# Optimization experiments

Hardware: AMD Instinct MI355X
Metric: run time of the kernel (lower is better)

Reference implementation:

```python
import jax, jax.numpy as jnp
import numpy as np

BETA = 1e10  # hard softmax temperature from the original module


def setup_inputs() -> dict:
    key = jax.random.key(0)
    ks = jax.random.split(key, 7)
    bs, nc, units, feat = 128, 1024, 512, 512
    return {
        "x": jax.random.normal(ks[0], (bs, feat), jnp.float32),
        "class_logits": jax.random.normal(ks[1], (bs, nc), jnp.float32),
        "h_states": jax.random.normal(ks[2], (nc, units), jnp.float32) * 0.1,
        "c_states": jax.random.normal(ks[3], (nc, units), jnp.float32) * 0.1,
        "kernel": jax.random.normal(ks[4], (feat, 4 * units), jnp.float32) * 0.05,
        "rec_kernel": jax.random.normal(ks[5], (units, 4 * units), jnp.float32) * 0.05,
        "bias": jnp.zeros((4 * units,), jnp.float32),
    }


def _diff_scatter(A, B, w):
    # A: (nc, u) old class states, B: (bs, u) new states, w: (bs, nc) hard softmax.
    # Faithful to tf version: broadcast to (nc, bs, u), blend, then reduce_max over bs.
    m = w.T[:, :, None]                       # (nc, bs, 1)
    blended = A[:, None, :] * (1.0 - m) + B[None, :, :] * m  # (nc, bs, u)
    return jnp.max(blended, axis=1)           # (nc, u)


def reference(x, class_logits, h_states, c_states, kernel, rec_kernel, bias):
    # diff_gather: softmax-weighted sum over classes == weights @ params
    w = jax.nn.softmax(class_logits * BETA, axis=-1)  # (bs, nc), ~one-hot
    h0 = w @ h_states                                  # (bs, u)
    c0 = w @ c_states                                  # (bs, u)

    # single-step Keras LSTM (seq_len == 1): gate order i, f, c, o
    z = x @ kernel + h0 @ rec_kernel + bias            # (bs, 4u)
    i, f, g, o = jnp.split(z, 4, axis=-1)
    i = jax.nn.sigmoid(i)
    f = jax.nn.sigmoid(f)
    g = jnp.tanh(g)
    o = jax.nn.sigmoid(o)
    c = f * c0 + i * g
    h = o * jnp.tanh(c)                                # LSTM output == h

    new_h = _diff_scatter(h_states, h, w)
    new_c = _diff_scatter(c_states, c, w)
    return h, new_h, new_c
```

## Files before the change

kernel.cpp:

```cpp
#include <hip/hip_runtime.h>
#include <hip/hip_bf16.h>
#include <math.h>

#define BS    128
#define NC    1024
#define UNITS 512
#define FEAT  512
#define FOURU 2048
#define KG    8

typedef short bf16x8 __attribute__((ext_vector_type(8)));
typedef float f32x4  __attribute__((ext_vector_type(4)));

__device__ __forceinline__ unsigned short bf_rhu(float f) {
    union { float f; unsigned u; } v; v.f = f;
    return (unsigned short)((v.u + 0x8000u) >> 16);
}
__device__ __forceinline__ unsigned pack2(float a, float b) {
    return (unsigned)bf_rhu(a) | ((unsigned)bf_rhu(b) << 16);
}

__global__ __launch_bounds__(256) void prep_kernel(
    const float* __restrict__ logits, const float* __restrict__ x,
    const float* __restrict__ h_st,
    const float* __restrict__ kern, const float* __restrict__ reck,
    int* __restrict__ sidx,
    unsigned short* __restrict__ Abf,
    unsigned short* __restrict__ Wt)
{
    const int bid = blockIdx.x, t = threadIdx.x;
    const int wid = t >> 6, lane = t & 63;

    if (bid < BS) {
        int b = bid;
        float best = -INFINITY; int bi = 0;
        for (int i = t; i < NC; i += 256) {
            float v = logits[b * NC + i];
            if (v > best) { best = v; bi = i; }
        }
        for (int off = 32; off > 0; off >>= 1) {
            float ov = __shfl_down(best, off);
            int   oi = __shfl_down(bi, off);
            if (ov > best || (ov == best && oi < bi)) { best = ov; bi = oi; }
        }
        __shared__ float sv[4]; __shared__ int si[4]; __shared__ int sbi;
        if ((t & 63) == 0) { sv[wid] = best; si[wid] = bi; }
        __syncthreads();
        if (t == 0) {
            for (int w = 1; w < 4; ++w)
                if (sv[w] > best || (sv[w] == best && si[w] < bi)) { best = sv[w]; bi = si[w]; }
            sidx[b] = bi;
            sbi = bi;
        }
        __syncthreads();
        int st = t & 127;
        const float* srcrow = (t < 128) ? (x + (long)b * FEAT)
                                        : (h_st + (long)sbi * UNITS);
        float4 v = *(const float4*)(srcrow + st * 4);
        unsigned lo = pack2(v.x, v.y), hi = pack2(v.z, v.w);
        unsigned du = (unsigned)b * 512u + (t < 128 ? 0u : 256u) + (unsigned)st * 2u;
        *(uint2*)((unsigned*)Abf + du) = make_uint2(lo, hi);
    } else {
        int gw = (bid - BS) * 4 + wid;
        for (int task = gw; task < 4096; task += 1536) {
            int kc = task >> 5;
            int n  = (task & 31) * 64 + lane;
            int r0 = kc * 8;
            const float* base = (r0 < 512) ? (kern + (long)r0 * FOURU + n)
                                           : (reck + (long)(r0 - 512) * FOURU + n);
            bf16x8 o;
            #pragma unroll
            for (int j = 0; j < 8; ++j)
                o[j] = (short)bf_rhu(base[(long)j * FOURU]);
            *(bf16x8*)(Wt + (long)n * 1024 + r0) = o;
        }
    }
}

__global__ __launch_bounds__(256) void gemm_kernel(
    const unsigned short* __restrict__ Abf,
    const unsigned short* __restrict__ Wt,
    float* __restrict__ z_part)
{
    const int t = threadIdx.x;
    const int wid = t >> 6, lane = t & 63, l15 = lane & 15, quad = lane >> 4;
    const int nt = blockIdx.x & 63, kg = blockIdx.x >> 6;
    const int k0base = kg * 128 + quad * 8;

    f32x4 zero = {0.f, 0.f, 0.f, 0.f};
    f32x4 acc[2][2] = {{zero, zero}, {zero, zero}};

    #pragma unroll
    for (int kstep = 0; kstep < 4; ++kstep) {
        int k0 = k0base + kstep * 32;
        bf16x8 af[2], wf[2];
        #pragma unroll
        for (int ms = 0; ms < 2; ++ms) {
            int m = wid * 32 + ms * 16 + l15;
            af[ms] = *(const bf16x8*)(Abf + (long)m * 1024 + k0);
        }
        #pragma unroll
        for (int ns = 0; ns < 2; ++ns) {
            int n = nt * 32 + ns * 16 + l15;
            wf[ns] = *(const bf16x8*)(Wt + (long)n * 1024 + k0);
        }
        #pragma unroll
        for (int ms = 0; ms < 2; ++ms)
            #pragma unroll
            for (int ns = 0; ns < 2; ++ns)
                acc[ms][ns] = __builtin_amdgcn_mfma_f32_16x16x32_bf16(
                                  af[ms], wf[ns], acc[ms][ns], 0, 0, 0);
    }

    float* zp = z_part + (long)kg * BS * FOURU;
    #pragma unroll
    for (int ms = 0; ms < 2; ++ms)
        #pragma unroll
        for (int ns = 0; ns < 2; ++ns)
            #pragma unroll
            for (int r = 0; r < 4; ++r) {
                int m = wid * 32 + ms * 16 + quad * 4 + r;
                int n = nt * 32 + ns * 16 + l15;
                zp[(long)m * FOURU + n] = acc[ms][ns][r];
            }
}

__global__ __launch_bounds__(256) void scatter_lstm_kernel(
    const float* __restrict__ z_part, const float* __restrict__ bias,
    const float* __restrict__ h_states, const float* __restrict__ c_states,
    const int* __restrict__ sidx,
    float* __restrict__ h_out, float* __restrict__ out_h, float* __restrict__ out_c)
{
    __shared__ int s[BS];
    int t = threadIdx.x;
    if (t < BS) s[t] = sidx[t];
    __syncthreads();
    int j = blockIdx.x >> 1;
    int u = (blockIdx.x & 1) * 256 + t;

    float ah = h_states[(long)j * UNITS + u];
    float ac = c_states[(long)j * UNITS + u];

    float mh = -INFINITY, mc = -INFINITY;
    int count = 0;
    float bi_ = bias[u], bf_ = bias[512 + u], bg_ = bias[1024 + u], bo_ = bias[1536 + u];

    for (int b = 0; b < BS; ++b) {
        if (s[b] == j) {
            ++count;
            float zi = bi_, zf = bf_, zg = bg_, zo = bo_;
            #pragma unroll
            for (int kg = 0; kg < KG; ++kg) {
                const float* zp = z_part + (long)kg * BS * FOURU + (long)b * FOURU;
                zi += zp[u];
                zf += zp[512 + u];
                zg += zp[1024 + u];
                zo += zp[1536 + u];
            }
            float ig = 1.f / (1.f + expf(-zi));
            float fg = 1.f / (1.f + expf(-zf));
            float gg = tanhf(zg);
            float og = 1.f / (1.f + expf(-zo));
            float c  = fg * ac + ig * gg;
            float h  = og * tanhf(c);
            h_out[(long)b * UNITS + u] = h;
            mh = fmaxf(mh, h);
            mc = fmaxf(mc, c);
        }
    }
    out_h[(long)j * UNITS + u] = (count == BS) ? mh : fmaxf(ah, mh);
    out_c[(long)j * UNITS + u] = (count == BS) ? mc : fmaxf(ac, mc);
}

extern "C" void kernel_launch(void* const* d_in, const int* in_sizes, int n_in,
                              void* d_out, int out_size, void* d_ws, size_t ws_size,
                              hipStream_t stream)
{
    (void)in_sizes; (void)n_in; (void)out_size; (void)ws_size;
    const float* x      = (const float*)d_in[0];
    const float* logits = (const float*)d_in[1];
    const float* h_st   = (const float*)d_in[2];
    const float* c_st   = (const float*)d_in[3];
    const float* kern   = (const float*)d_in[4];
    const float* reck   = (const float*)d_in[5];
    const float* bias   = (const float*)d_in[6];

    float* out        = (float*)d_out;
    float* out_h_step = out;
    float* out_newh   = out + BS * UNITS;
    float* out_newc   = out + BS * UNITS + NC * UNITS;

    char*           ws     = (char*)d_ws;
    int*            sidx   = (int*)ws;
    unsigned short* Abf    = (unsigned short*)(ws + 4096);
    float*          z_part = (float*)(ws + (1u << 20));
    unsigned short* Wt     = (unsigned short*)(ws + 10u * (1u << 20));

    prep_kernel<<<512, 256, 0, stream>>>(logits, x, h_st, kern, reck, sidx, Abf, Wt);
    gemm_kernel<<<512, 256, 0, stream>>>(Abf, Wt, z_part);
    scatter_lstm_kernel<<<NC * UNITS / 256, 256, 0, stream>>>(
        z_part, bias, h_st, c_st, sidx, out_h_step, out_newh, out_newc);
}
```

Baseline: 103.3 us.

## Fuse weight bf16 conversion into GEMM loads and drop transposed weight buffer

Removes the separate pass that converts kernel/rec_kernel into a transposed bf16 buffer. The GEMM now reads fp32 weights directly and converts them in registers while building MFMA fragments. The grid changes to 128 N-tiles of 16 columns by 4 K-groups of 256, which halves the split-K partials the scatter kernel must sum. This saves a full write and re-read of the 8 MB weight copy, at the cost of strided fp32 loads and fewer MFMAs per loaded A fragment.

```diff
diff --git a/kernel.cpp b/kernel.cpp
--- a/kernel.cpp
+++ b/kernel.cpp
@@ -7,7 +7,8 @@
 #define UNITS 512
 #define FEAT  512
 #define FOURU 2048
-#define KG    8
+#define KG    4
+#define NT    16
 
 typedef short bf16x8 __attribute__((ext_vector_type(8)));
 typedef float f32x4  __attribute__((ext_vector_type(4)));
@@ -20,109 +21,88 @@
     return (unsigned)bf_rhu(a) | ((unsigned)bf_rhu(b) << 16);
 }
 
-__global__ __launch_bounds__(256) void prep_kernel(
+__global__ __launch_bounds__(256) void argmax_prep_kernel(
     const float* __restrict__ logits, const float* __restrict__ x,
-    const float* __restrict__ h_st,
-    const float* __restrict__ kern, const float* __restrict__ reck,
-    int* __restrict__ sidx,
-    unsigned short* __restrict__ Abf,
-    unsigned short* __restrict__ Wt)
+    const float* __restrict__ h_states,
+    int* __restrict__ sidx, unsigned* __restrict__ Abf )
 {
-    const int bid = blockIdx.x, t = threadIdx.x;
-    const int wid = t >> 6, lane = t & 63;
-
-    if (bid < BS) {
-        int b = bid;
-        float best = -INFINITY; int bi = 0;
-        for (int i = t; i < NC; i += 256) {
-            float v = logits[b * NC + i];
-            if (v > best) { best = v; bi = i; }
-        }
-        for (int off = 32; off > 0; off >>= 1) {
-            float ov = __shfl_down(best, off);
-            int   oi = __shfl_down(bi, off);
-            if (ov > best || (ov == best && oi < bi)) { best = ov; bi = oi; }
-        }
-        __shared__ float sv[4]; __shared__ int si[4]; __shared__ int sbi;
-        if ((t & 63) == 0) { sv[wid] = best; si[wid] = bi; }
-        __syncthreads();
-        if (t == 0) {
-            for (int w = 1; w < 4; ++w)
-                if (sv[w] > best || (sv[w] == best && si[w] < bi)) { best = sv[w]; bi = si[w]; }
-            sidx[b] = bi;
-            sbi = bi;
-        }
-        __syncthreads();
-        int st = t & 127;
-        const float* srcrow = (t < 128) ? (x + (long)b * FEAT)
-                                        : (h_st + (long)sbi * UNITS);
-        float4 v = *(const float4*)(srcrow + st * 4);
-        unsigned lo = pack2(v.x, v.y), hi = pack2(v.z, v.w);
-        unsigned du = (unsigned)b * 512u + (t < 128 ? 0u : 256u) + (unsigned)st * 2u;
-        *(uint2*)((unsigned*)Abf + du) = make_uint2(lo, hi);
-    } else {
-        int gw = (bid - BS) * 4 + wid;
-        for (int task = gw; task < 4096; task += 1536) {
-            int kc = task >> 5;
-            int n  = (task & 31) * 64 + lane;
-            int r0 = kc * 8;
-            const float* base = (r0 < 512) ? (kern + (long)r0 * FOURU + n)
-                                           : (reck + (long)(r0 - 512) * FOURU + n);
-            bf16x8 o;
-            #pragma unroll
-            for (int j = 0; j < 8; ++j)
-                o[j] = (short)bf_rhu(base[(long)j * FOURU]);
-            *(bf16x8*)(Wt + (long)n * 1024 + r0) = o;
-        }
+    int b = blockIdx.x;
+    int t = threadIdx.x;
+    float best = -INFINITY; int bi = 0;
+    for (int i = t; i < NC; i += 256) {
+        float v = logits[b * NC + i];
+        if (v > best) { best = v; bi = i; }
     }
+    for (int off = 32; off > 0; off >>= 1) {
+        float ov = __shfl_down(best, off);
+        int   oi = __shfl_down(bi, off);
+        if (ov > best || (ov == best && oi < bi)) { best = ov; bi = oi; }
+    }
+    __shared__ float sv[4]; __shared__ int si[4]; __shared__ int sbi;
+    int wid = t >> 6;
+    if ((t & 63) == 0) { sv[wid] = best; si[wid] = bi; }
+    __syncthreads();
+    if (t == 0) {
+        for (int w = 1; w < 4; ++w)
+            if (sv[w] > best || (sv[w] == best && si[w] < bi)) { best = sv[w]; bi = si[w]; }
+        sidx[b] = bi;
+        sbi = bi;
+    }
+    __syncthreads();
+    int st = t & 127;
+    const float* srcrow = (t < 128) ? (x + (long)b * FEAT)
+                                    : (h_states + (long)sbi * UNITS);
+    float4 v = *(const float4*)(srcrow + st * 4);
+    unsigned lo = pack2(v.x, v.y), hi = pack2(v.z, v.w);
+    unsigned du = (unsigned)b * 512u + (t < 128 ? 0u : 256u) + (unsigned)st * 2u;
+    *(uint2*)(Abf + du) = make_uint2(lo, hi);
 }
 
 __global__ __launch_bounds__(256) void gemm_kernel(
     const unsigned short* __restrict__ Abf,
-    const unsigned short* __restrict__ Wt,
+    const float* __restrict__ kern, const float* __restrict__ reck,
     float* __restrict__ z_part)
 {
     const int t = threadIdx.x;
     const int wid = t >> 6, lane = t & 63, l15 = lane & 15, quad = lane >> 4;
-    const int nt = blockIdx.x & 63, kg = blockIdx.x >> 6;
-    const int k0base = kg * 128 + quad * 8;
+    const int nt = blockIdx.x, kg = blockIdx.y;
+    const int n  = nt * NT + l15;
+    const int k0base = kg * 256;
+    const float* W  = (kg < 2) ? kern : reck;
+    const int wkbase = (kg & 1) * 256;
 
     f32x4 zero = {0.f, 0.f, 0.f, 0.f};
-    f32x4 acc[2][2] = {{zero, zero}, {zero, zero}};
+    f32x4 acc[2] = {zero, zero};
 
     #pragma unroll
-    for (int kstep = 0; kstep < 4; ++kstep) {
-        int k0 = k0base + kstep * 32;
-        bf16x8 af[2], wf[2];
+    for (int kstep = 0; kstep < 8; ++kstep) {
+        int k0  = k0base + kstep * 32 + quad * 8;
+        int wk0 = wkbase + kstep * 32 + quad * 8;
+
+        bf16x8 af[2], wf;
         #pragma unroll
         for (int ms = 0; ms < 2; ++ms) {
             int m = wid * 32 + ms * 16 + l15;
             af[ms] = *(const bf16x8*)(Abf + (long)m * 1024 + k0);
         }
+        const float* Wp = W + (long)wk0 * FOURU + n;
         #pragma unroll
-        for (int ns = 0; ns < 2; ++ns) {
-            int n = nt * 32 + ns * 16 + l15;
-            wf[ns] = *(const bf16x8*)(Wt + (long)n * 1024 + k0);
-        }
+        for (int j = 0; j < 8; ++j)
+            wf[j] = (short)bf_rhu(Wp[(long)j * FOURU]);
+
         #pragma unroll
         for (int ms = 0; ms < 2; ++ms)
-            #pragma unroll
-            for (int ns = 0; ns < 2; ++ns)
-                acc[ms][ns] = __builtin_amdgcn_mfma_f32_16x16x32_bf16(
-                                  af[ms], wf[ns], acc[ms][ns], 0, 0, 0);
+            acc[ms] = __builtin_amdgcn_mfma_f32_16x16x32_bf16(af[ms], wf, acc[ms], 0, 0, 0);
     }
 
     float* zp = z_part + (long)kg * BS * FOURU;
     #pragma unroll
     for (int ms = 0; ms < 2; ++ms)
         #pragma unroll
-        for (int ns = 0; ns < 2; ++ns)
-            #pragma unroll
-            for (int r = 0; r < 4; ++r) {
-                int m = wid * 32 + ms * 16 + quad * 4 + r;
-                int n = nt * 32 + ns * 16 + l15;
-                zp[(long)m * FOURU + n] = acc[ms][ns][r];
-            }
+        for (int r = 0; r < 4; ++r) {
+            int m = wid * 32 + ms * 16 + quad * 4 + r;
+            zp[(long)m * FOURU + n] = acc[ms][r];
+        }
 }
 
 __global__ __launch_bounds__(256) void scatter_lstm_kernel(
@@ -192,12 +172,12 @@
 
     char*           ws     = (char*)d_ws;
     int*            sidx   = (int*)ws;
-    unsigned short* Abf    = (unsigned short*)(ws + 4096);
+    unsigned*       Abf    = (unsigned*)(ws + 4096);
     float*          z_part = (float*)(ws + (1u << 20));
-    unsigned short* Wt     = (unsigned short*)(ws + 10u * (1u << 20));
 
-    prep_kernel<<<512, 256, 0, stream>>>(logits, x, h_st, kern, reck, sidx, Abf, Wt);
-    gemm_kernel<<<512, 256, 0, stream>>>(Abf, Wt, z_part);
+    argmax_prep_kernel<<<BS, 256, 0, stream>>>(logits, x, h_st, sidx, Abf);
+    gemm_kernel<<<dim3(128, KG), 256, 0, stream>>>(
+        (const unsigned short*)Abf, kern, reck, z_part);
     scatter_lstm_kernel<<<NC * UNITS / 256, 256, 0, stream>>>(
         z_part, bias, h_st, c_st, sidx, out_h_step, out_newh, out_newc);
 }
```

New measurement: 103.3 us, median of 2. Within noise of the previous version (+0.0%).
